# Kernel tuning notes

Measured on AMD Instinct MI355X. Metric: run time of the kernel, lower is better.

## Reference

```python
import jax, jax.numpy as jnp
import numpy as np

N, E, IN_CH, HID, HEADS, OUT = 50000, 800000, 128, 64, 2, 64
NEG_SLOPE = 0.2

def setup_inputs() -> dict:
    key = jax.random.key(0)
    ks = jax.random.split(key, 10)
    return {
        "x": jax.random.normal(ks[0], (N, IN_CH), dtype=jnp.float32),
        "edge_index": jax.random.randint(ks[1], (2, E), 0, N, dtype=jnp.int32),
        "W1": jax.random.normal(ks[2], (HEADS * HID, IN_CH), dtype=jnp.float32) * 0.05,
        "att1_src": jax.random.normal(ks[3], (HEADS, HID), dtype=jnp.float32) * 0.05,
        "att1_dst": jax.random.normal(ks[4], (HEADS, HID), dtype=jnp.float32) * 0.05,
        "b1": jax.random.normal(ks[5], (HEADS * HID,), dtype=jnp.float32) * 0.05,
        "W2": jax.random.normal(ks[6], (OUT, HEADS * HID), dtype=jnp.float32) * 0.05,
        "att2_src": jax.random.normal(ks[7], (1, OUT), dtype=jnp.float32) * 0.05,
        "att2_dst": jax.random.normal(ks[8], (1, OUT), dtype=jnp.float32) * 0.05,
        "b2": jax.random.normal(ks[9], (OUT,), dtype=jnp.float32) * 0.05,
    }

def _gat_conv(x, src, dst, W, a_src, a_dst, b, heads, out_ch, concat, n):
    # linear transform -> [N, H, C]
    h = (x @ W.T).reshape(n, heads, out_ch)
    # per-node attention halves: [N, H]
    alpha_s = (h * a_src[None]).sum(-1)
    alpha_d = (h * a_dst[None]).sum(-1)
    # per-edge raw score (messages flow src -> dst): [E, H]
    e = jax.nn.leaky_relu(alpha_s[src] + alpha_d[dst], negative_slope=NEG_SLOPE)
    # scatter-softmax normalized over each destination neighborhood
    m = jax.ops.segment_max(e, dst, num_segments=n)
    ex = jnp.exp(e - m[dst])
    denom = jax.ops.segment_sum(ex, dst, num_segments=n)
    alpha = ex / (denom[dst] + 1e-16)
    # weighted scatter-add of source features: [N, H, C]
    out = jax.ops.segment_sum(h[src] * alpha[:, :, None], dst, num_segments=n)
    out = out.reshape(n, heads * out_ch) if concat else out.mean(axis=1)
    return out + b

def reference(x, edge_index, W1, att1_src, att1_dst, b1, W2, att2_src, att2_dst, b2):
    n = x.shape[0]
    # PyG GATConv adds self-loops by default
    loops = jnp.arange(n, dtype=edge_index.dtype)
    src = jnp.concatenate([edge_index[0], loops])
    dst = jnp.concatenate([edge_index[1], loops])
    # dropout layers inactive (eval mode)
    h = _gat_conv(x, src, dst, W1, att1_src, att1_dst, b1, HEADS, HID, True, n)
    h = jax.nn.elu(h)
    out = _gat_conv(h, src, dst, W2, att2_src, att2_dst, b2, 1, OUT, False, n)
    return out
```

## Files before the change

kernel.cpp:

```cpp
#include <hip/hip_runtime.h>
#include <hip/hip_bf16.h>
#include <math.h>

typedef __bf16 bf16x8 __attribute__((ext_vector_type(8)));
typedef float f32x4 __attribute__((ext_vector_type(4)));
typedef float f32x2 __attribute__((ext_vector_type(2)));

__device__ __forceinline__ float lrelu(float x) { return x > 0.f ? x : 0.2f * x; }
__device__ __forceinline__ unsigned short f2bf(float f) {
    unsigned u = __float_as_uint(f);
    return (unsigned short)((u + 0x7fffu + ((u >> 16) & 1u)) >> 16);
}
__device__ __forceinline__ float bf16lo(unsigned u) { return __uint_as_float(u << 16); }
__device__ __forceinline__ float bf16hi(unsigned u) { return __uint_as_float(u & 0xffff0000u); }
__device__ __forceinline__ unsigned pkbf(float a, float b) {
    return (unsigned)f2bf(a) | ((unsigned)f2bf(b) << 16);
}
__device__ __forceinline__ float wred_sum(float v) {
#pragma unroll
    for (int o = 32; o; o >>= 1) v += __shfl_xor(v, o);
    return v;
}

__global__ __launch_bounds__(256) void cast_w(const float* __restrict__ W1,
                                              const float* __restrict__ W2,
                                              unsigned short* __restrict__ w1b,
                                              unsigned short* __restrict__ w2b) {
    int i = blockIdx.x * 256 + threadIdx.x;
    const float* src;
    unsigned short* dst;
    size_t off;
    if (i < 2048)      { src = W1; dst = w1b; off = (size_t)i * 8; }
    else if (i < 3072) { src = W2; dst = w2b; off = (size_t)(i - 2048) * 8; }
    else return;
    float4 v0 = *(const float4*)(src + off);
    float4 v1 = *(const float4*)(src + off + 4);
    union { unsigned short u[8]; uint4 q; } o;
    o.u[0] = f2bf(v0.x); o.u[1] = f2bf(v0.y); o.u[2] = f2bf(v0.z); o.u[3] = f2bf(v0.w);
    o.u[4] = f2bf(v1.x); o.u[5] = f2bf(v1.y); o.u[6] = f2bf(v1.z); o.u[7] = f2bf(v1.w);
    *(uint4*)(dst + off) = o.q;
}

__global__ __launch_bounds__(256) void k1_hist(const int* __restrict__ ei, int E, int Et,
                                               int* __restrict__ g_hist, int NB) {
    __shared__ int hist[256];
    int tid = threadIdx.x, b = blockIdx.x;
    hist[tid] = 0;
    __syncthreads();
    int base = b * 4096;
#pragma unroll
    for (int k = 0; k < 16; ++k) {
        int e = base + k * 256 + tid;
        if (e < Et) {
            int d = (e < E) ? ei[E + e] : (e - E);
            atomicAdd(&hist[d >> 8], 1);
        }
    }
    __syncthreads();
    g_hist[tid * NB + b] = hist[tid];
}

__global__ __launch_bounds__(256) void scan_p1(const int* __restrict__ in,
                                               int* __restrict__ partial, int n) {
    __shared__ int ws[4];
    int tid = threadIdx.x, lane = tid & 63, w = tid >> 6;
    int idx = blockIdx.x * 256 + tid;
    int v = (idx < n) ? in[idx] : 0;
    int s = v;
#pragma unroll
    for (int o = 32; o; o >>= 1) s += __shfl_xor(s, o);
    if (lane == 0) ws[w] = s;
    __syncthreads();
    if (tid == 0) partial[blockIdx.x] = ws[0] + ws[1] + ws[2] + ws[3];
}

__global__ __launch_bounds__(256) void scan_p2(int* __restrict__ partial, int nb) {
    __shared__ int ws[4];
    __shared__ int s_carry;
    int tid = threadIdx.x, lane = tid & 63, w = tid >> 6;
    if (tid == 0) s_carry = 0;
    __syncthreads();
    for (int base = 0; base < nb; base += 256) {
        int idx = base + tid;
        int v = (idx < nb) ? partial[idx] : 0;
        int incl = v;
#pragma unroll
        for (int off = 1; off < 64; off <<= 1) {
            int t = __shfl_up(incl, off);
            if (lane >= off) incl += t;
        }
        if (lane == 63) ws[w] = incl;
        __syncthreads();
        int wpre = 0;
        for (int k = 0; k < w; ++k) wpre += ws[k];
        int carry = s_carry;
        if (idx < nb) partial[idx] = carry + wpre + incl - v;
        __syncthreads();
        if (tid == 255) s_carry = carry + wpre + incl;
        __syncthreads();
    }
}

__global__ __launch_bounds__(256) void scan_p3g(const int* __restrict__ in,
                                                const int* __restrict__ partial,
                                                int* __restrict__ out, int n) {
    __shared__ int ws[4];
    int tid = threadIdx.x, lane = tid & 63, w = tid >> 6;
    int idx = blockIdx.x * 256 + tid;
    int v = (idx < n) ? in[idx] : 0;
    int incl = v;
#pragma unroll
    for (int off = 1; off < 64; off <<= 1) {
        int t = __shfl_up(incl, off);
        if (lane >= off) incl += t;
    }
    if (lane == 63) ws[w] = incl;
    __syncthreads();
    int wpre = 0;
    for (int k = 0; k < w; ++k) wpre += ws[k];
    if (idx < n) out[idx] = partial[blockIdx.x] + wpre + incl - v;
    if (idx == n - 1) out[n] = partial[blockIdx.x] + wpre + incl;
}

__global__ __launch_bounds__(256) void k3_scatter(const int* __restrict__ ei, int E, int Et,
                                                  const int* __restrict__ g_scan,
                                                  uint2* __restrict__ tmp, int NB) {
    __shared__ int hist[256], lofs[256], lcnt[256], gbase[256];
    __shared__ int ws4[4];
    __shared__ uint2 stage[4096];
    int tid = threadIdx.x, b = blockIdx.x;
    int lane = tid & 63, w = tid >> 6;
    int base = b * 4096;
    int valid = min(4096, Et - base);
    uint2 ev[16];
    hist[tid] = 0;
    lcnt[tid] = 0;
    gbase[tid] = g_scan[tid * NB + b];
    __syncthreads();
#pragma unroll
    for (int k = 0; k < 16; ++k) {
        int e = base + k * 256 + tid;
        if (e < Et) {
            int s, d;
            if (e < E) { s = ei[e]; d = ei[E + e]; } else { s = d = e - E; }
            ev[k] = make_uint2((unsigned)d, (unsigned)s);
            atomicAdd(&hist[d >> 8], 1);
        }
    }
    __syncthreads();
    {
        int v = hist[tid];
        int incl = v;
#pragma unroll
        for (int off = 1; off < 64; off <<= 1) {
            int t = __shfl_up(incl, off);
            if (lane >= off) incl += t;
        }
        if (lane == 63) ws4[w] = incl;
        __syncthreads();
        int wpre = 0;
        for (int k = 0; k < w; ++k) wpre += ws4[k];
        lofs[tid] = wpre + incl - v;
    }
    __syncthreads();
#pragma unroll
    for (int k = 0; k < 16; ++k) {
        int e = base + k * 256 + tid;
        if (e < Et) {
            int dg = ev[k].x >> 8;
            int r = atomicAdd(&lcnt[dg], 1);
            stage[lofs[dg] + r] = ev[k];
        }
    }
    __syncthreads();
    for (int j = tid; j < valid; j += 256) {
        uint2 v = stage[j];
        int dg = v.x >> 8;
        tmp[gbase[dg] + (j - lofs[dg])] = v;
    }
}

__global__ __launch_bounds__(256) void csr_finalize(const uint2* __restrict__ tmp,
                                                    const int* __restrict__ g_scan,
                                                    int* __restrict__ srcs,
                                                    int* __restrict__ rowptr,
                                                    int N, int Et, int NB) {
    __shared__ int cnt[256], lofs[256], lcnt[256];
    __shared__ int ws4[4];
    int tid = threadIdx.x, g = blockIdx.x;
    int lane = tid & 63, w = tid >> 6;
    int start = g_scan[g * NB];
    int end = g_scan[(g + 1) * NB];
    cnt[tid] = 0;
    lcnt[tid] = 0;
    __syncthreads();
    for (int e = start + tid; e < end; e += 256)
        atomicAdd(&cnt[tmp[e].x & 255u], 1);
    __syncthreads();
    {
        int v = cnt[tid];
        int incl = v;
#pragma unroll
        for (int off = 1; off < 64; off <<= 1) {
            int t = __shfl_up(incl, off);
            if (lane >= off) incl += t;
        }
        if (lane == 63) ws4[w] = incl;
        __syncthreads();
        int wpre = 0;
        for (int k = 0; k < w; ++k) wpre += ws4[k];
        lofs[tid] = wpre + incl - v;
    }
    __syncthreads();
    int d = g * 256 + tid;
    if (d < N) rowptr[d] = start + lofs[tid];
    if (d == N - 1) rowptr[N] = Et;
    for (int e = start + tid; e < end; e += 256) {
        uint2 v = tmp[e];
        int sub = v.x & 255u;
        int pos = start + lofs[sub] + atomicAdd(&lcnt[sub], 1);
        srcs[pos] = (int)v.y;
    }
}

template<int M, int H, bool AF32>
__global__ __launch_bounds__(256) void gemm_mfma(const void* __restrict__ Av,
                                                 const unsigned short* __restrict__ Wb,
                                                 const float* __restrict__ att_s,
                                                 const float* __restrict__ att_d,
                                                 unsigned short* __restrict__ Cb,
                                                 float* __restrict__ as_,
                                                 float* __restrict__ ad_,
                                                 int N) {
    constexpr int CT = M / 16;
    int tid = threadIdx.x;
    int wid = tid >> 6, l = tid & 63;
    int l15 = l & 15, lhi = l >> 4;
    int rowbase = blockIdx.x * 64 + wid * 16;
    f32x4 acc[CT] = {};

    int rc = min(rowbase + l15, N - 1);
    const unsigned short* ap = (const unsigned short*)Av + (size_t)rc * 128 + lhi * 8;
    const float* apf = (const float*)Av + (size_t)rc * 128 + lhi * 8;
    const unsigned short* wp = Wb + (size_t)l15 * 128 + lhi * 8;

#pragma unroll
    for (int ks = 0; ks < 4; ++ks) {
        int k0 = ks * 32;
        bf16x8 a;
        if (AF32) {
            float4 u0 = *(const float4*)(apf + k0);
            float4 u1 = *(const float4*)(apf + k0 + 4);
            union { unsigned short s[8]; bf16x8 v; } cc;
            cc.s[0] = f2bf(u0.x); cc.s[1] = f2bf(u0.y); cc.s[2] = f2bf(u0.z); cc.s[3] = f2bf(u0.w);
            cc.s[4] = f2bf(u1.x); cc.s[5] = f2bf(u1.y); cc.s[6] = f2bf(u1.z); cc.s[7] = f2bf(u1.w);
            a = cc.v;
        } else {
            a = *reinterpret_cast<const bf16x8*>(ap + k0);
        }
#pragma unroll
        for (int ct = 0; ct < CT; ++ct) {
            bf16x8 b = *reinterpret_cast<const bf16x8*>(wp + (size_t)ct * 16 * 128 + k0);
            acc[ct] = __builtin_amdgcn_mfma_f32_16x16x32_bf16(a, b, acc[ct], 0, 0, 0);
        }
    }

    int rbase = rowbase + lhi * 4;
#pragma unroll
    for (int j = 0; j < 4; ++j) {
        int gr = rbase + j;
        if (gr < N) {
#pragma unroll
            for (int ct = 0; ct < CT; ++ct)
                Cb[(size_t)gr * M + ct * 16 + l15] = f2bf(acc[ct][j]);
        }
    }
#pragma unroll
    for (int hd = 0; hd < H; ++hd) {
        float ps0 = 0.f, ps1 = 0.f, ps2 = 0.f, ps3 = 0.f;
        float pd0 = 0.f, pd1 = 0.f, pd2 = 0.f, pd3 = 0.f;
#pragma unroll
        for (int c4 = 0; c4 < 4; ++c4) {
            int ct = hd * 4 + c4;
            float ws = att_s[hd * 64 + c4 * 16 + l15];
            float wd = att_d[hd * 64 + c4 * 16 + l15];
            ps0 += acc[ct][0] * ws; pd0 += acc[ct][0] * wd;
            ps1 += acc[ct][1] * ws; pd1 += acc[ct][1] * wd;
            ps2 += acc[ct][2] * ws; pd2 += acc[ct][2] * wd;
            ps3 += acc[ct][3] * ws; pd3 += acc[ct][3] * wd;
        }
#pragma unroll
        for (int o = 1; o < 16; o <<= 1) {
            ps0 += __shfl_xor(ps0, o); pd0 += __shfl_xor(pd0, o);
            ps1 += __shfl_xor(ps1, o); pd1 += __shfl_xor(pd1, o);
            ps2 += __shfl_xor(ps2, o); pd2 += __shfl_xor(pd2, o);
            ps3 += __shfl_xor(ps3, o); pd3 += __shfl_xor(pd3, o);
        }
        if (l15 == 0) {
            int gr = rbase;
            if (gr < N)     { as_[(size_t)gr * H + hd] = ps0; ad_[(size_t)gr * H + hd] = pd0; }
            if (gr + 1 < N) { as_[(size_t)(gr + 1) * H + hd] = ps1; ad_[(size_t)(gr + 1) * H + hd] = pd1; }
            if (gr + 2 < N) { as_[(size_t)(gr + 2) * H + hd] = ps2; ad_[(size_t)(gr + 2) * H + hd] = pd2; }
            if (gr + 3 < N) { as_[(size_t)(gr + 3) * H + hd] = ps3; ad_[(size_t)(gr + 3) * H + hd] = pd3; }
        }
    }
}

template<int H, bool DO_ELU>
__global__ __launch_bounds__(256) void gat_agg(const int* __restrict__ rowptr,
                                               const int* __restrict__ srcs,
                                               const float* __restrict__ as_,
                                               const float* __restrict__ ad_,
                                               const unsigned* __restrict__ hfeat,
                                               const float* __restrict__ bias,
                                               void* __restrict__ outp, int N) {
    constexpr int RW = 32 * H;
    constexpr int G  = (H == 2) ? 4 : 8;
    constexpr int GL = 64 / G;
    __shared__ uint4 sent[4][64];
    int wid = threadIdx.x >> 6, lane = threadIdx.x & 63;
    int il = lane & (GL - 1);
    int grp = lane >> ((H == 2) ? 4 : 3);
    int d = blockIdx.x * 4 + wid;
    if (d >= N) return;
    int r0 = rowptr[d], r1 = rowptr[d + 1];
    int cnt = r1 - r0;
    float uad[H];
    if (H == 2) {
        float2 adp = *(const float2*)(ad_ + 2 * (size_t)d);
        uad[0] = adp.x; uad[H - 1] = adp.y;
    } else {
        uad[0] = ad_[d];
    }
    f32x2 A01 = {0.f, 0.f}, A23 = {0.f, 0.f}, A45 = {0.f, 0.f}, A67 = {0.f, 0.f};
    const char* hflb = (const char*)hfeat + 16 * il;
    bool hhi = (H == 2) && (il >= 8);
    const unsigned* sbase = reinterpret_cast<const unsigned*>(&sent[wid][0]) + (hhi ? 2 : 0);

    if (cnt <= 64) {
        int i = r0 + lane;
        bool act = i < r1;
        int se = act ? srcs[i] : 0;
        float ax[H];
        if (H == 2) {
            float2 asp = *(const float2*)(as_ + 2 * (size_t)se);
            float ex0 = act ? __expf(lrelu(asp.x + uad[0])) : 0.f;
            float ex1 = act ? __expf(lrelu(asp.y + uad[1])) : 0.f;
            float den0 = wred_sum(ex0);
            float den1 = wred_sum(ex1);
            ax[0] = ex0 * __builtin_amdgcn_rcpf(den0 + 1e-16f);
            ax[H - 1] = ex1 * __builtin_amdgcn_rcpf(den1 + 1e-16f);
        } else {
            float ex = act ? __expf(lrelu(as_[se] + uad[0])) : 0.f;
            float den = wred_sum(ex);
            ax[0] = ex * __builtin_amdgcn_rcpf(den + 1e-16f);
        }
        unsigned off = (unsigned)(se * (RW * 4));
        sent[wid][lane] = make_uint4(off, __float_as_uint(ax[0]),
                                     off, __float_as_uint(ax[H - 1]));
        __threadfence_block();
#pragma unroll 2
        for (int t = 0; t < cnt; t += G) {
            uint2 en = *(const uint2*)(sbase + 4 * (t + grp));
            float af = __uint_as_float(en.y);
            uint4 u = *(const uint4*)(hflb + en.x);
            f32x2 c;
            c.x = bf16lo(u.x); c.y = bf16hi(u.x); A01 += af * c;
            c.x = bf16lo(u.y); c.y = bf16hi(u.y); A23 += af * c;
            c.x = bf16lo(u.z); c.y = bf16hi(u.z); A45 += af * c;
            c.x = bf16lo(u.w); c.y = bf16hi(u.w); A67 += af * c;
        }
    } else {
        float psum[H];
#pragma unroll
        for (int h = 0; h < H; ++h) psum[h] = 0.f;
        for (int base = r0; base < r1; base += 64) {
            int i = base + lane;
            bool act = i < r1;
            int s = act ? srcs[i] : 0;
#pragma unroll
            for (int h = 0; h < H; ++h) {
                float sc = lrelu(as_[(size_t)s * H + h] + uad[h]);
                psum[h] += act ? __expf(sc) : 0.f;
            }
        }
        float inv[H];
#pragma unroll
        for (int h = 0; h < H; ++h)
            inv[h] = __builtin_amdgcn_rcpf(wred_sum(psum[h]) + 1e-16f);
        for (int base = r0; base < r1; base += 64) {
            int i = base + lane;
            bool act = i < r1;
            int se = act ? srcs[i] : 0;
            float ax[H];
#pragma unroll
            for (int h = 0; h < H; ++h) {
                float sc = lrelu(as_[(size_t)se * H + h] + uad[h]);
                ax[h] = act ? __expf(sc) * inv[h] : 0.f;
            }
            int cntc = min(64, r1 - base);
            unsigned off = (unsigned)(se * (RW * 4));
            sent[wid][lane] = make_uint4(off, __float_as_uint(ax[0]),
                                         off, __float_as_uint(ax[H - 1]));
            __threadfence_block();
            for (int t = 0; t < cntc; t += G) {
                uint2 en = *(const uint2*)(sbase + 4 * (t + grp));
                float af = __uint_as_float(en.y);
                uint4 u = *(const uint4*)(hflb + en.x);
                f32x2 c;
                c.x = bf16lo(u.x); c.y = bf16hi(u.x); A01 += af * c;
                c.x = bf16lo(u.y); c.y = bf16hi(u.y); A23 += af * c;
                c.x = bf16lo(u.z); c.y = bf16hi(u.z); A45 += af * c;
                c.x = bf16lo(u.w); c.y = bf16hi(u.w); A67 += af * c;
            }
            __threadfence_block();
        }
    }

#pragma unroll
    for (int o = GL; o < 64; o <<= 1) {
        A01.x += __shfl_xor(A01.x, o); A01.y += __shfl_xor(A01.y, o);
        A23.x += __shfl_xor(A23.x, o); A23.y += __shfl_xor(A23.y, o);
        A45.x += __shfl_xor(A45.x, o); A45.y += __shfl_xor(A45.y, o);
        A67.x += __shfl_xor(A67.x, o); A67.y += __shfl_xor(A67.y, o);
    }
    if (grp == 0) {
        int c0 = 8 * il;
        float4 bA = *(const float4*)(bias + c0);
        float4 bB = *(const float4*)(bias + c0 + 4);
        float v0 = A01.x + bA.x, v1 = A01.y + bA.y, v2 = A23.x + bA.z, v3 = A23.y + bA.w;
        float v4 = A45.x + bB.x, v5 = A45.y + bB.y, v6 = A67.x + bB.z, v7 = A67.y + bB.w;
        if (DO_ELU) {
            v0 = v0 > 0.f ? v0 : expm1f(v0); v1 = v1 > 0.f ? v1 : expm1f(v1);
            v2 = v2 > 0.f ? v2 : expm1f(v2); v3 = v3 > 0.f ? v3 : expm1f(v3);
            v4 = v4 > 0.f ? v4 : expm1f(v4); v5 = v5 > 0.f ? v5 : expm1f(v5);
            v6 = v6 > 0.f ? v6 : expm1f(v6); v7 = v7 > 0.f ? v7 : expm1f(v7);
        }
        if (H == 2) {
            uint4 o;
            o.x = pkbf(v0, v1); o.y = pkbf(v2, v3);
            o.z = pkbf(v4, v5); o.w = pkbf(v6, v7);
            *(uint4*)((unsigned*)outp + (size_t)d * 64 + 4 * il) = o;
        } else {
            *(float4*)((float*)outp + (size_t)d * 64 + c0) = make_float4(v0, v1, v2, v3);
            *(float4*)((float*)outp + (size_t)d * 64 + c0 + 4) = make_float4(v4, v5, v6, v7);
        }
    }
}

extern "C" void kernel_launch(void* const* d_in, const int* in_sizes, int n_in,
                              void* d_out, int out_size, void* d_ws, size_t ws_size,
                              hipStream_t stream) {
    const float* x   = (const float*)d_in[0];
    const int*   ei  = (const int*)d_in[1];
    const float* W1  = (const float*)d_in[2];
    const float* a1s = (const float*)d_in[3];
    const float* a1d = (const float*)d_in[4];
    const float* b1  = (const float*)d_in[5];
    const float* W2  = (const float*)d_in[6];
    const float* a2s = (const float*)d_in[7];
    const float* a2d = (const float*)d_in[8];
    const float* b2  = (const float*)d_in[9];
    float* out = (float*)d_out;

    int N  = in_sizes[0] / 128;
    int E  = in_sizes[1] / 2;
    int Et = E + N;
    int NB = (Et + 4095) / 4096;
    int nh = 256 * NB;

    char* p = (char*)d_ws;
    unsigned short* h1b = (unsigned short*)p;   p += (size_t)N * 128 * 2;
    unsigned short* act1b = (unsigned short*)p; p += (size_t)N * 128 * 2;
    unsigned short* h2b = (unsigned short*)p;   p += (size_t)N * 64 * 2;
    unsigned short* w1b = (unsigned short*)p;   p += 128 * 128 * 2;
    unsigned short* w2b = (unsigned short*)p;   p += 64 * 128 * 2;
    uint2* tmp = (uint2*)p;                p += (size_t)Et * 8;
    int* g_hist = (int*)p;                 p += (size_t)nh * 4;
    int* g_scan = (int*)p;                 p += (size_t)(nh + 1) * 4;
    int* partial = (int*)p;                p += (size_t)((nh + 255) / 256) * 4;
    float* as1 = (float*)p;                p += (size_t)N * 2 * 4;
    float* ad1 = (float*)p;                p += (size_t)N * 2 * 4;
    float* as2 = (float*)p;                p += (size_t)N * 4;
    float* ad2 = (float*)p;                p += (size_t)N * 4;
    int* rowptr = (int*)p;                 p += (size_t)(N + 1) * 4;
    int* srcs = (int*)p;                   p += (size_t)Et * 4;

    int nbs = (nh + 255) / 256;
    k1_hist<<<NB, 256, 0, stream>>>(ei, E, Et, g_hist, NB);
    scan_p1<<<nbs, 256, 0, stream>>>(g_hist, partial, nh);
    scan_p2<<<1, 256, 0, stream>>>(partial, nbs);
    scan_p3g<<<nbs, 256, 0, stream>>>(g_hist, partial, g_scan, nh);
    k3_scatter<<<NB, 256, 0, stream>>>(ei, E, Et, g_scan, tmp, NB);
    csr_finalize<<<256, 256, 0, stream>>>(tmp, g_scan, srcs, rowptr, N, Et, NB);

    cast_w<<<12, 256, 0, stream>>>(W1, W2, w1b, w2b);

    gemm_mfma<128, 2, true><<<(N + 63) / 64, 256, 0, stream>>>(x, w1b, a1s, a1d, h1b, as1, ad1, N);
    gat_agg<2, true><<<(N + 3) / 4, 256, 0, stream>>>(rowptr, srcs, as1, ad1,
                                                      (const unsigned*)h1b, b1, act1b, N);

    gemm_mfma<64, 1, false><<<(N + 63) / 64, 256, 0, stream>>>(act1b, w2b, a2s, a2d, h2b, as2, ad2, N);
    gat_agg<1, false><<<(N + 3) / 4, 256, 0, stream>>>(rowptr, srcs, as2, ad2,
                                                       (const unsigned*)h2b, b2, out, N);
}
```

Before: 143.6 us.

## Pack CSR edge pairs into 32 bits, fold weight cast, widen aggregation lanes

Folds the bf16 weight-cast kernel into the histogram kernel as extra blocks, which removes one launch. Packs each (dst, src) edge pair into a single 32-bit word instead of a uint2, halving scatter and temporary traffic during CSR construction. This relies on node ids fitting in 16 bits, so it only holds while N stays below 65536. csr_finalize now stages each bucket's source indices in LDS before a coalesced write-out, falling back to direct writes when a bucket exceeds 8192 edges. For the two-head layer, the aggregation kernel now uses 8 edge groups per wavefront, with each lane reading 32 bytes of features per edge, in place of 4 groups reading 16 bytes.

```diff
diff --git a/kernel.cpp b/kernel.cpp
--- a/kernel.cpp
+++ b/kernel.cpp
@@ -22,29 +22,31 @@
     return v;
 }
 
-__global__ __launch_bounds__(256) void cast_w(const float* __restrict__ W1,
-                                              const float* __restrict__ W2,
-                                              unsigned short* __restrict__ w1b,
-                                              unsigned short* __restrict__ w2b) {
-    int i = blockIdx.x * 256 + threadIdx.x;
-    const float* src;
-    unsigned short* dst;
-    size_t off;
-    if (i < 2048)      { src = W1; dst = w1b; off = (size_t)i * 8; }
-    else if (i < 3072) { src = W2; dst = w2b; off = (size_t)(i - 2048) * 8; }
-    else return;
-    float4 v0 = *(const float4*)(src + off);
-    float4 v1 = *(const float4*)(src + off + 4);
-    union { unsigned short u[8]; uint4 q; } o;
-    o.u[0] = f2bf(v0.x); o.u[1] = f2bf(v0.y); o.u[2] = f2bf(v0.z); o.u[3] = f2bf(v0.w);
-    o.u[4] = f2bf(v1.x); o.u[5] = f2bf(v1.y); o.u[6] = f2bf(v1.z); o.u[7] = f2bf(v1.w);
-    *(uint4*)(dst + off) = o.q;
-}
 
 __global__ __launch_bounds__(256) void k1_hist(const int* __restrict__ ei, int E, int Et,
-                                               int* __restrict__ g_hist, int NB) {
+                                               int* __restrict__ g_hist, int NB,
+                                               const float* __restrict__ W1,
+                                               const float* __restrict__ W2,
+                                               unsigned short* __restrict__ w1b,
+                                               unsigned short* __restrict__ w2b) {
+    int tid = threadIdx.x, b = blockIdx.x;
+    if (b >= NB) {
+        int i = (b - NB) * 256 + tid;
+        const float* src;
+        unsigned short* dst;
+        size_t off;
+        if (i < 2048)      { src = W1; dst = w1b; off = (size_t)i * 8; }
+        else if (i < 3072) { src = W2; dst = w2b; off = (size_t)(i - 2048) * 8; }
+        else return;
+        float4 v0 = *(const float4*)(src + off);
+        float4 v1 = *(const float4*)(src + off + 4);
+        union { unsigned short u[8]; uint4 q; } o;
+        o.u[0] = f2bf(v0.x); o.u[1] = f2bf(v0.y); o.u[2] = f2bf(v0.z); o.u[3] = f2bf(v0.w);
+        o.u[4] = f2bf(v1.x); o.u[5] = f2bf(v1.y); o.u[6] = f2bf(v1.z); o.u[7] = f2bf(v1.w);
+        *(uint4*)(dst + off) = o.q;
+        return;
+    }
     __shared__ int hist[256];
-    int tid = threadIdx.x, b = blockIdx.x;
     hist[tid] = 0;
     __syncthreads();
     int base = b * 4096;
@@ -124,15 +126,15 @@
 
 __global__ __launch_bounds__(256) void k3_scatter(const int* __restrict__ ei, int E, int Et,
                                                   const int* __restrict__ g_scan,
-                                                  uint2* __restrict__ tmp, int NB) {
+                                                  unsigned* __restrict__ tmp, int NB) {
     __shared__ int hist[256], lofs[256], lcnt[256], gbase[256];
     __shared__ int ws4[4];
-    __shared__ uint2 stage[4096];
+    __shared__ unsigned stage[4096];
     int tid = threadIdx.x, b = blockIdx.x;
     int lane = tid & 63, w = tid >> 6;
     int base = b * 4096;
     int valid = min(4096, Et - base);
-    uint2 ev[16];
+    unsigned pv[16];
     hist[tid] = 0;
     lcnt[tid] = 0;
     gbase[tid] = g_scan[tid * NB + b];
@@ -143,7 +145,7 @@
         if (e < Et) {
             int s, d;
             if (e < E) { s = ei[e]; d = ei[E + e]; } else { s = d = e - E; }
-            ev[k] = make_uint2((unsigned)d, (unsigned)s);
+            pv[k] = ((unsigned)d << 16) | (unsigned)s;
             atomicAdd(&hist[d >> 8], 1);
         }
     }
@@ -167,35 +169,37 @@
     for (int k = 0; k < 16; ++k) {
         int e = base + k * 256 + tid;
         if (e < Et) {
-            int dg = ev[k].x >> 8;
+            int dg = pv[k] >> 24;
             int r = atomicAdd(&lcnt[dg], 1);
-            stage[lofs[dg] + r] = ev[k];
+            stage[lofs[dg] + r] = pv[k];
         }
     }
     __syncthreads();
     for (int j = tid; j < valid; j += 256) {
-        uint2 v = stage[j];
-        int dg = v.x >> 8;
+        unsigned v = stage[j];
+        int dg = v >> 24;
         tmp[gbase[dg] + (j - lofs[dg])] = v;
     }
 }
 
-__global__ __launch_bounds__(256) void csr_finalize(const uint2* __restrict__ tmp,
+__global__ __launch_bounds__(256) void csr_finalize(const unsigned* __restrict__ tmp,
                                                     const int* __restrict__ g_scan,
                                                     int* __restrict__ srcs,
                                                     int* __restrict__ rowptr,
                                                     int N, int Et, int NB) {
     __shared__ int cnt[256], lofs[256], lcnt[256];
     __shared__ int ws4[4];
+    __shared__ unsigned short sstage[8192];
     int tid = threadIdx.x, g = blockIdx.x;
     int lane = tid & 63, w = tid >> 6;
     int start = g_scan[g * NB];
     int end = g_scan[(g + 1) * NB];
+    int sz = end - start;
     cnt[tid] = 0;
     lcnt[tid] = 0;
     __syncthreads();
     for (int e = start + tid; e < end; e += 256)
-        atomicAdd(&cnt[tmp[e].x & 255u], 1);
+        atomicAdd(&cnt[(tmp[e] >> 16) & 255u], 1);
     __syncthreads();
     {
         int v = cnt[tid];
@@ -215,11 +219,23 @@
     int d = g * 256 + tid;
     if (d < N) rowptr[d] = start + lofs[tid];
     if (d == N - 1) rowptr[N] = Et;
-    for (int e = start + tid; e < end; e += 256) {
-        uint2 v = tmp[e];
-        int sub = v.x & 255u;
-        int pos = start + lofs[sub] + atomicAdd(&lcnt[sub], 1);
-        srcs[pos] = (int)v.y;
+    if (sz <= 8192) {
+        for (int e = start + tid; e < end; e += 256) {
+            unsigned v = tmp[e];
+            int sub = (v >> 16) & 255u;
+            int pos = lofs[sub] + atomicAdd(&lcnt[sub], 1);
+            sstage[pos] = (unsigned short)(v & 0xffffu);
+        }
+        __syncthreads();
+        for (int j = tid; j < sz; j += 256)
+            srcs[start + j] = (int)sstage[j];
+    } else {
+        for (int e = start + tid; e < end; e += 256) {
+            unsigned v = tmp[e];
+            int sub = (v >> 16) & 255u;
+            int pos = start + lofs[sub] + atomicAdd(&lcnt[sub], 1);
+            srcs[pos] = (int)(v & 0xffffu);
+        }
     }
 }
 
@@ -315,12 +331,12 @@
                                                const float* __restrict__ bias,
                                                void* __restrict__ outp, int N) {
     constexpr int RW = 32 * H;
-    constexpr int G  = (H == 2) ? 4 : 8;
-    constexpr int GL = 64 / G;
+    constexpr int G  = 8;
+    constexpr int NV = 4 * H;
     __shared__ uint4 sent[4][64];
     int wid = threadIdx.x >> 6, lane = threadIdx.x & 63;
-    int il = lane & (GL - 1);
-    int grp = lane >> ((H == 2) ? 4 : 3);
+    int il = lane & 7;
+    int grp = lane >> 3;
     int d = blockIdx.x * 4 + wid;
     if (d >= N) return;
     int r0 = rowptr[d], r1 = rowptr[d + 1];
@@ -332,9 +348,11 @@
     } else {
         uad[0] = ad_[d];
     }
-    f32x2 A01 = {0.f, 0.f}, A23 = {0.f, 0.f}, A45 = {0.f, 0.f}, A67 = {0.f, 0.f};
-    const char* hflb = (const char*)hfeat + 16 * il;
-    bool hhi = (H == 2) && (il >= 8);
+    f32x2 A[NV];
+#pragma unroll
+    for (int q = 0; q < NV; ++q) A[q] = f32x2{0.f, 0.f};
+    const char* hflb = (const char*)hfeat + 16 * H * il;
+    bool hhi = (H == 2) && (il >= 4);
     const unsigned* sbase = reinterpret_cast<const unsigned*>(&sent[wid][0]) + (hhi ? 2 : 0);
 
     if (cnt <= 64) {
@@ -363,12 +381,20 @@
         for (int t = 0; t < cnt; t += G) {
             uint2 en = *(const uint2*)(sbase + 4 * (t + grp));
             float af = __uint_as_float(en.y);
-            uint4 u = *(const uint4*)(hflb + en.x);
+            const char* rowp = hflb + en.x;
+            uint4 u0 = *(const uint4*)(rowp);
             f32x2 c;
-            c.x = bf16lo(u.x); c.y = bf16hi(u.x); A01 += af * c;
-            c.x = bf16lo(u.y); c.y = bf16hi(u.y); A23 += af * c;
-            c.x = bf16lo(u.z); c.y = bf16hi(u.z); A45 += af * c;
-            c.x = bf16lo(u.w); c.y = bf16hi(u.w); A67 += af * c;
+            c.x = bf16lo(u0.x); c.y = bf16hi(u0.x); A[0] += af * c;
+            c.x = bf16lo(u0.y); c.y = bf16hi(u0.y); A[1] += af * c;
+            c.x = bf16lo(u0.z); c.y = bf16hi(u0.z); A[2] += af * c;
+            c.x = bf16lo(u0.w); c.y = bf16hi(u0.w); A[3] += af * c;
+            if (H == 2) {
+                uint4 u1 = *(const uint4*)(rowp + 16);
+                c.x = bf16lo(u1.x); c.y = bf16hi(u1.x); A[4] += af * c;
+                c.x = bf16lo(u1.y); c.y = bf16hi(u1.y); A[5] += af * c;
+                c.x = bf16lo(u1.z); c.y = bf16hi(u1.z); A[6] += af * c;
+                c.x = bf16lo(u1.w); c.y = bf16hi(u1.w); A[7] += af * c;
+            }
         }
     } else {
         float psum[H];
@@ -406,44 +432,59 @@
             for (int t = 0; t < cntc; t += G) {
                 uint2 en = *(const uint2*)(sbase + 4 * (t + grp));
                 float af = __uint_as_float(en.y);
-                uint4 u = *(const uint4*)(hflb + en.x);
+                const char* rowp = hflb + en.x;
+                uint4 u0 = *(const uint4*)(rowp);
                 f32x2 c;
-                c.x = bf16lo(u.x); c.y = bf16hi(u.x); A01 += af * c;
-                c.x = bf16lo(u.y); c.y = bf16hi(u.y); A23 += af * c;
-                c.x = bf16lo(u.z); c.y = bf16hi(u.z); A45 += af * c;
-                c.x = bf16lo(u.w); c.y = bf16hi(u.w); A67 += af * c;
+                c.x = bf16lo(u0.x); c.y = bf16hi(u0.x); A[0] += af * c;
+                c.x = bf16lo(u0.y); c.y = bf16hi(u0.y); A[1] += af * c;
+                c.x = bf16lo(u0.z); c.y = bf16hi(u0.z); A[2] += af * c;
+                c.x = bf16lo(u0.w); c.y = bf16hi(u0.w); A[3] += af * c;
+                if (H == 2) {
+                    uint4 u1 = *(const uint4*)(rowp + 16);
+                    c.x = bf16lo(u1.x); c.y = bf16hi(u1.x); A[4] += af * c;
+                    c.x = bf16lo(u1.y); c.y = bf16hi(u1.y); A[5] += af * c;
+                    c.x = bf16lo(u1.z); c.y = bf16hi(u1.z); A[6] += af * c;
+                    c.x = bf16lo(u1.w); c.y = bf16hi(u1.w); A[7] += af * c;
+                }
             }
             __threadfence_block();
         }
     }
 
 #pragma unroll
-    for (int o = GL; o < 64; o <<= 1) {
-        A01.x += __shfl_xor(A01.x, o); A01.y += __shfl_xor(A01.y, o);
-        A23.x += __shfl_xor(A23.x, o); A23.y += __shfl_xor(A23.y, o);
-        A45.x += __shfl_xor(A45.x, o); A45.y += __shfl_xor(A45.y, o);
-        A67.x += __shfl_xor(A67.x, o); A67.y += __shfl_xor(A67.y, o);
+    for (int o = 8; o < 64; o <<= 1) {
+#pragma unroll
+        for (int q = 0; q < NV; ++q) {
+            A[q].x += __shfl_xor(A[q].x, o);
+            A[q].y += __shfl_xor(A[q].y, o);
+        }
     }
     if (grp == 0) {
-        int c0 = 8 * il;
-        float4 bA = *(const float4*)(bias + c0);
-        float4 bB = *(const float4*)(bias + c0 + 4);
-        float v0 = A01.x + bA.x, v1 = A01.y + bA.y, v2 = A23.x + bA.z, v3 = A23.y + bA.w;
-        float v4 = A45.x + bB.x, v5 = A45.y + bB.y, v6 = A67.x + bB.z, v7 = A67.y + bB.w;
+        int c0 = 8 * H * il;
+        float v[2 * NV];
+#pragma unroll
+        for (int q = 0; q < NV; ++q) {
+            float2 bq = *(const float2*)(bias + c0 + 2 * q);
+            v[2 * q]     = A[q].x + bq.x;
+            v[2 * q + 1] = A[q].y + bq.y;
+        }
         if (DO_ELU) {
-            v0 = v0 > 0.f ? v0 : expm1f(v0); v1 = v1 > 0.f ? v1 : expm1f(v1);
-            v2 = v2 > 0.f ? v2 : expm1f(v2); v3 = v3 > 0.f ? v3 : expm1f(v3);
-            v4 = v4 > 0.f ? v4 : expm1f(v4); v5 = v5 > 0.f ? v5 : expm1f(v5);
-            v6 = v6 > 0.f ? v6 : expm1f(v6); v7 = v7 > 0.f ? v7 : expm1f(v7);
+#pragma unroll
+            for (int q = 0; q < 2 * NV; ++q) v[q] = v[q] > 0.f ? v[q] : expm1f(v[q]);
         }
         if (H == 2) {
-            uint4 o;
-            o.x = pkbf(v0, v1); o.y = pkbf(v2, v3);
-            o.z = pkbf(v4, v5); o.w = pkbf(v6, v7);
-            *(uint4*)((unsigned*)outp + (size_t)d * 64 + 4 * il) = o;
+            uint4 o1, o2;
+            o1.x = pkbf(v[0], v[1]);  o1.y = pkbf(v[2], v[3]);
+            o1.z = pkbf(v[4], v[5]);  o1.w = pkbf(v[6], v[7]);
+            o2.x = pkbf(v[8], v[9]);  o2.y = pkbf(v[10], v[11]);
+            o2.z = pkbf(v[12], v[13]); o2.w = pkbf(v[14], v[15]);
+            unsigned* ob = (unsigned*)outp + (size_t)d * 64 + 8 * il;
+            *(uint4*)ob = o1;
+            *(uint4*)(ob + 4) = o2;
         } else {
-            *(float4*)((float*)outp + (size_t)d * 64 + c0) = make_float4(v0, v1, v2, v3);
-            *(float4*)((float*)outp + (size_t)d * 64 + c0 + 4) = make_float4(v4, v5, v6, v7);
+            float* ob = (float*)outp + (size_t)d * 64 + c0;
+            *(float4*)ob = make_float4(v[0], v[1], v[2], v[3]);
+            *(float4*)(ob + 4) = make_float4(v[4], v[5], v[6], v[7]);
         }
     }
 }
@@ -475,7 +516,7 @@
     unsigned short* h2b = (unsigned short*)p;   p += (size_t)N * 64 * 2;
     unsigned short* w1b = (unsigned short*)p;   p += 128 * 128 * 2;
     unsigned short* w2b = (unsigned short*)p;   p += 64 * 128 * 2;
-    uint2* tmp = (uint2*)p;                p += (size_t)Et * 8;
+    unsigned* tmp = (unsigned*)p;          p += (size_t)Et * 4;
     int* g_hist = (int*)p;                 p += (size_t)nh * 4;
     int* g_scan = (int*)p;                 p += (size_t)(nh + 1) * 4;
     int* partial = (int*)p;                p += (size_t)((nh + 255) / 256) * 4;
@@ -487,15 +528,13 @@
     int* srcs = (int*)p;                   p += (size_t)Et * 4;
 
     int nbs = (nh + 255) / 256;
-    k1_hist<<<NB, 256, 0, stream>>>(ei, E, Et, g_hist, NB);
+    k1_hist<<<NB + 12, 256, 0, stream>>>(ei, E, Et, g_hist, NB, W1, W2, w1b, w2b);
     scan_p1<<<nbs, 256, 0, stream>>>(g_hist, partial, nh);
     scan_p2<<<1, 256, 0, stream>>>(partial, nbs);
     scan_p3g<<<nbs, 256, 0, stream>>>(g_hist, partial, g_scan, nh);
     k3_scatter<<<NB, 256, 0, stream>>>(ei, E, Et, g_scan, tmp, NB);
     csr_finalize<<<256, 256, 0, stream>>>(tmp, g_scan, srcs, rowptr, N, Et, NB);
 
-    cast_w<<<12, 256, 0, stream>>>(W1, W2, w1b, w2b);
-
     gemm_mfma<128, 2, true><<<(N + 63) / 64, 256, 0, stream>>>(x, w1b, a1s, a1d, h1b, as1, ad1, N);
     gat_agg<2, true><<<(N + 3) / 4, 256, 0, stream>>>(rowptr, srcs, as1, ad1,
                                                       (const unsigned*)h1b, b1, act1b, N);
```

After: 154.4 us. 7.6% more time.
